# Kernel tuning notes

Measured on AMD Instinct MI355X. Metric: run time of the kernel, lower is better.

## Reference

```python
import jax, jax.numpy as jnp
import numpy as np

B, T, J, V, D, H = 32, 400, 30, 50000, 150, 150
L = 2  # answer_token_len (boundary model: start, end)


def _gru_step(h, x, Wih, Whh, bih, bhh):
    # torch GRUCell semantics
    gi = x @ Wih.T + bih
    gh = h @ Whh.T + bhh
    ir, iz, inn = jnp.split(gi, 3, axis=-1)
    hr, hz, hn = jnp.split(gh, 3, axis=-1)
    r = jax.nn.sigmoid(ir + hr)
    z = jax.nn.sigmoid(iz + hz)
    n = jnp.tanh(inn + r * hn)
    return (1.0 - z) * n + z * h


def _gru_seq(x, Wih, Whh, bih, bhh):
    # x: [B, S, din] -> hidden sequence [B, S, h]
    h0 = jnp.zeros((x.shape[0], Whh.shape[1]), x.dtype)
    def step(h, xt):
        h = _gru_step(h, xt, Wih, Whh, bih, bhh)
        return h, h
    _, hs = jax.lax.scan(step, h0, jnp.swapaxes(x, 0, 1))
    return jnp.swapaxes(hs, 0, 1)


def _forward(context, query,
             E,
             ctx_Wih, ctx_Whh, ctx_bih, ctx_bhh,
             q_Wih, q_Whh, q_bih, q_bhh,
             Wq, Wp, Wr, w, gate_bias, attn_bias,
             m_Wih, m_Whh, m_bih, m_bhh,
             mr_Wih, mr_Whh, mr_bih, mr_bhh,
             ptr_W1, ptr_W2, ptr_v,
             d_Wih, d_Whh, d_bih, d_bhh):
    # encode context and query with GRUs
    Hp = _gru_seq(E[context], ctx_Wih, ctx_Whh, ctx_bih, ctx_bhh)  # [B,T,H]
    Hq = _gru_seq(E[query], q_Wih, q_Whh, q_bih, q_bhh)            # [B,J,H]

    whq = jnp.einsum('bjh,hk->bjk', Hq, Wq)  # precomputed query projection [B,J,H]

    def match_scan(xs, cWih, cWhh, cbih, cbhh):
        # xs: [B,T,H] context encodings (possibly time-reversed)
        def step(h, xt):
            # G_i = tanh(Wq Hq + (Wp p_i + Wr h_{i-1}) + bias)  -> [B,J,H]
            g = jnp.tanh(whq + (xt @ Wp + h @ Wr + gate_bias)[:, None, :])
            a = jax.nn.softmax(g @ w + attn_bias, axis=-1)       # [B,J]
            q = jnp.einsum('bj,bjh->bh', a, Hq)                  # attended query
            z = jnp.concatenate([xt, q], axis=-1)                # [B,2H]
            h = _gru_step(h, z, cWih, cWhh, cbih, cbhh)
            return h, h
        h0 = jnp.zeros((xs.shape[0], xs.shape[2]), xs.dtype)
        _, hs = jax.lax.scan(step, h0, jnp.swapaxes(xs, 0, 1))
        return jnp.swapaxes(hs, 0, 1)  # [B,T,H]

    Hf = match_scan(Hp, m_Wih, m_Whh, m_bih, m_bhh)              # forward direction
    Hb = match_scan(Hp[:, ::-1], mr_Wih, mr_Whh, mr_bih, mr_bhh) # reverse direction (scan order, as original)
    Hr = jnp.concatenate([Hf, Hb], axis=-1)                      # [B,T,2H]
    zero0 = jnp.zeros((Hr.shape[0], 1, Hr.shape[2]), Hr.dtype)   # initial zero state prepended
    Hr = jnp.concatenate([zero0, Hr], axis=1)                    # [B,T+1,2H]

    # boundary pointer network: L attention steps over H_r
    enc = Hr @ ptr_W1
    def ptr_step(h, _):
        s = jnp.tanh(enc + (h @ ptr_W2)[:, None, :]) @ ptr_v     # [B,T+1]
        a = jax.nn.softmax(s, axis=-1)
        c = jnp.einsum('bt,bth->bh', a, Hr)
        h = _gru_step(h, c, d_Wih, d_Whh, d_bih, d_bhh)
        return h, a
    h0 = jnp.zeros((Hr.shape[0], Hr.shape[2]), Hr.dtype)
    _, probs = jax.lax.scan(ptr_step, h0, None, length=L)
    return jnp.swapaxes(probs, 0, 1)  # [B, L, T+1]


def setup_inputs() -> dict:
    key = jax.random.key(0)
    keys = iter(jax.random.split(key, 40))
    p = lambda *s: jax.random.normal(next(keys), s, jnp.float32) * 0.05
    inp = {
        'context': jax.random.randint(next(keys), (B, T), 0, V, dtype=jnp.int32),
        'query': jax.random.randint(next(keys), (B, J), 0, V, dtype=jnp.int32),
        'E': p(V, D),
        'ctx_Wih': p(3 * H, D), 'ctx_Whh': p(3 * H, H), 'ctx_bih': p(3 * H), 'ctx_bhh': p(3 * H),
        'q_Wih': p(3 * H, D), 'q_Whh': p(3 * H, H), 'q_bih': p(3 * H), 'q_bhh': p(3 * H),
        'Wq': p(H, H), 'Wp': p(H, H), 'Wr': p(H, H), 'w': p(H),
        'gate_bias': p(H), 'attn_bias': p(),
        'm_Wih': p(3 * H, 2 * H), 'm_Whh': p(3 * H, H), 'm_bih': p(3 * H), 'm_bhh': p(3 * H),
        'mr_Wih': p(3 * H, 2 * H), 'mr_Whh': p(3 * H, H), 'mr_bih': p(3 * H), 'mr_bhh': p(3 * H),
        'ptr_W1': p(2 * H, 2 * H), 'ptr_W2': p(2 * H, 2 * H), 'ptr_v': p(2 * H),
        'd_Wih': p(6 * H, 2 * H), 'd_Whh': p(6 * H, 2 * H), 'd_bih': p(6 * H), 'd_bhh': p(6 * H),
    }
    return inp


def reference(context, query, E,
              ctx_Wih, ctx_Whh, ctx_bih, ctx_bhh,
              q_Wih, q_Whh, q_bih, q_bhh,
              Wq, Wp, Wr, w, gate_bias, attn_bias,
              m_Wih, m_Whh, m_bih, m_bhh,
              mr_Wih, mr_Whh, mr_bih, mr_bhh,
              ptr_W1, ptr_W2, ptr_v,
              d_Wih, d_Whh, d_bih, d_bhh):
    return _forward(context, query, E,
                    ctx_Wih, ctx_Whh, ctx_bih, ctx_bhh,
                    q_Wih, q_Whh, q_bih, q_bhh,
                    Wq, Wp, Wr, w, gate_bias, attn_bias,
                    m_Wih, m_Whh, m_bih, m_bhh,
                    mr_Wih, mr_Whh, mr_bih, mr_bhh,
                    ptr_W1, ptr_W2, ptr_v,
                    d_Wih, d_Whh, d_bih, d_bhh)
```

## Files before the change

### kernel.cpp

```cpp
#include <hip/hip_runtime.h>
#include <hip/hip_bf16.h>


namespace {

constexpr int NBATCH = 32;
constexpr int TLEN   = 400;
constexpr int JQ     = 30;
constexpr int T1     = 401;

__device__ __forceinline__ float sigm(float x){ return 1.f/(1.f+__expf(-x)); }
__device__ __forceinline__ float tanh_f(float x){
  float e = __expf(-2.f*fabsf(x));
  float t = (1.f-e)/(1.f+e);
  return x < 0.f ? -t : t;
}
__device__ __forceinline__ float bf2f(unsigned short u){
  union { unsigned int i; float f; } c; c.i = ((unsigned int)u)<<16; return c.f;
}
__device__ __forceinline__ float q4max(float4 v){ return fmaxf(fmaxf(v.x,v.y),fmaxf(v.z,v.w)); }
__device__ __forceinline__ float sum4(float4 v){ return (v.x+v.y)+(v.z+v.w); }
__device__ __forceinline__ float4 exp4(float4 v, float m){
  return make_float4(__expf(v.x-m),__expf(v.y-m),__expf(v.z-m),__expf(v.w-m));
}
__device__ __forceinline__ float4 scl4(float4 v, float s){
  return make_float4(v.x*s,v.y*s,v.z*s,v.w*s);
}

__device__ __forceinline__ void bar_lds(){
  asm volatile("s_waitcnt lgkmcnt(0)" ::: "memory");
  __builtin_amdgcn_s_barrier();
}

#define NW 29
struct WDesc { const void* src[NW]; int off[NW+1]; };

__global__ void sniff_kernel(const unsigned int* __restrict__ bits, int* __restrict__ flag){
  __shared__ int cnt;
  if (threadIdx.x==0) cnt = 0;
  __syncthreads();
  int hit = 0;
  #pragma unroll
  for (int i=0;i<4;i++){
    unsigned int w = bits[threadIdx.x*4+i];
    unsigned int b = (w>>8)&0x7Fu;
    if (b==0u || (b>=0x38u && b<=0x3Fu)) hit++;
  }
  atomicAdd(&cnt, hit);
  __syncthreads();
  if (threadIdx.x==0) *flag = (cnt > 768) ? 1 : 0;
}

__global__ void convert_weights_kernel(WDesc d, float* __restrict__ out, const int* __restrict__ flag){
  const int isbf = *flag;
  const int total = d.off[NW];
  for (int e = blockIdx.x*blockDim.x+threadIdx.x; e < total; e += gridDim.x*blockDim.x){
    int j = 0;
    while (e >= d.off[j+1]) j++;
    int i = e - d.off[j];
    out[e] = isbf ? bf2f(((const unsigned short*)d.src[j])[i])
                  : ((const float*)d.src[j])[i];
  }
}

struct PrepArgs {
  const float *ctxWhh, *qWhh, *mWhh, *mrWhh, *Wr;
  const float *ctxWih, *qWih, *mWih, *mrWih;
  float *ctxWhhP, *qWhhP, *s2qCtx, *s2qQ, *WcatF, *WcatR, *s2qF, *s2qR;
  float *extF, *extR, *ctxWihT, *qWihT, *mXfT, *mXrT, *mQfT, *mQrT;
};

__global__ void prep_all_kernel(PrepArgs a){
  const int PN[16] = {68400,68400,21696,21696,91200,91200,24576,24576,
                      13376,13376,67500,67500,67500,67500,67500,67500};
  const int TOT = 843496;
  for (int gid = blockIdx.x*blockDim.x+threadIdx.x; gid < TOT; gid += gridDim.x*blockDim.x){
    int e = gid, t = 0;
    while (e >= PN[t]){ e -= PN[t]; t++; }
    switch (t){
      case 0: case 1: {
        const float* s = (t==0)? a.ctxWhh : a.qWhh;
        float* d = (t==0)? a.ctxWhhP : a.qWhhP;
        int r = e/152, c = e-r*152;
        d[e] = (c<150) ? s[r*150+c] : 0.f;
      } break;
      case 2: case 3: {
        const float* s = (t==2)? a.ctxWhh : a.qWhh;
        float* d = (t==2)? a.s2qCtx : a.s2qQ;
        int q = e/1808, rem = e-q*1808, r = rem/4, p = rem-r*4;
        int c = 104 + 4*q + p;
        d[e] = (r<450 && c<150) ? s[(size_t)r*150+c] : 0.f;
      } break;
      case 4: case 5: {
        const float* s = (t==4)? a.mWhh : a.mrWhh;
        float* d = (t==4)? a.WcatF : a.WcatR;
        int r = e/152, c = e-r*152;
        float v = 0.f;
        if (c < 150) v = (r<450) ? s[(size_t)r*150+c] : a.Wr[(size_t)c*150 + (r-450)];
        d[e] = v;
      } break;
      case 6: case 7: {
        const float* s = (t==6)? a.mWhh : a.mrWhh;
        float* d = (t==6)? a.s2qF : a.s2qR;
        int q = e/2048, rem = e-q*2048, r = rem/4, p = rem-r*4;
        int c = 104 + 4*q + p;
        float v = 0.f;
        if (c < 150) v = (r<450) ? s[(size_t)r*150+c] : a.Wr[(size_t)c*150 + (r-450)];
        d[e] = v;
      } break;
      case 8: case 9: {
        float* d = (t==8)? a.extF : a.extR;
        int q = e/352, rem = e-q*352, ii = rem/4, p = rem-ii*4;
        int c = 4*q + p;
        d[e] = (c<150) ? a.Wr[(size_t)c*150 + 62 + ii] : 0.f;
      } break;
      default: {
        int i2 = e/450, k = e-i2*450;
        const float* s; float* d; int lds_, offs;
        switch (t){
          case 10: s=a.ctxWih; d=a.ctxWihT; lds_=150; offs=0;   break;
          case 11: s=a.qWih;   d=a.qWihT;   lds_=150; offs=0;   break;
          case 12: s=a.mWih;   d=a.mXfT;    lds_=300; offs=0;   break;
          case 13: s=a.mrWih;  d=a.mXrT;    lds_=300; offs=0;   break;
          case 14: s=a.mWih;   d=a.mQfT;    lds_=300; offs=150; break;
          default: s=a.mrWih;  d=a.mQrT;    lds_=300; offs=150; break;
        }
        d[(size_t)i2*450 + k] = s[(size_t)k*lds_ + offs + i2];
      } break;
    }
  }
}

__global__ __launch_bounds__(512) void rowproj16_kernel(
    const float* __restrict__ Xrows,
    const int* __restrict__ gather, const void* __restrict__ Etab, const int* __restrict__ bfflag,
    const float* __restrict__ W, const float* __restrict__ bias,
    float* __restrict__ out, int rows, int K, int inner, int ldw, int ldo)
{
  __shared__ __align__(16) float xs[16][304];
  const int r0 = blockIdx.x*16;
  int nr = rows - r0; if (nr > 16) nr = 16;
  if (nr <= 0) return;
  const int isbf = gather ? *bfflag : 0;
  for (int e = threadIdx.x; e < nr*inner; e += 512){
    int r = e/inner, i = e - r*inner;
    float v;
    if (gather){
      size_t base = (size_t)gather[r0+r]*inner + i;
      v = isbf ? bf2f(((const unsigned short*)Etab)[base]) : ((const float*)Etab)[base];
    } else {
      v = Xrows[(size_t)(r0+r)*inner + i];
    }
    xs[r][i] = v;
  }
  __syncthreads();
  for (int k = threadIdx.x; k < K; k += 512){
    float b0 = bias ? bias[k] : 0.f;
    float acc[16];
    #pragma unroll
    for (int r=0;r<16;r++) acc[r] = b0;
    int i = 0;
    for (; i+4 <= inner; i += 4){
      float w0 = W[(size_t)i*ldw + k];
      float w1 = W[(size_t)(i+1)*ldw + k];
      float w2 = W[(size_t)(i+2)*ldw + k];
      float w3 = W[(size_t)(i+3)*ldw + k];
      #pragma unroll
      for (int r=0;r<16;r++){
        float4 xv = *(const float4*)&xs[r][i];
        acc[r] = fmaf(xv.x, w0, acc[r]);
        acc[r] = fmaf(xv.y, w1, acc[r]);
        acc[r] = fmaf(xv.z, w2, acc[r]);
        acc[r] = fmaf(xv.w, w3, acc[r]);
      }
    }
    for (; i < inner; i++){
      float wv = W[(size_t)i*ldw + k];
      #pragma unroll
      for (int r=0;r<16;r++) acc[r] = fmaf(xs[r][i], wv, acc[r]);
    }
    for (int r=0;r<nr;r++) out[(size_t)(r0+r)*ldo + k] = acc[r];
  }
  for (int k = K + threadIdx.x; k < ldo; k += 512)
    for (int r=0;r<nr;r++) out[(size_t)(r0+r)*ldo + k] = 0.f;
}

__device__ __forceinline__ void rowproj_one(
    const float xs[16][152], int nr, int r0,
    const float* __restrict__ W, const float* __restrict__ bias,
    float* __restrict__ out, int K, int ldw, int ldo)
{
  for (int k = threadIdx.x; k < K; k += 512){
    float b0 = bias ? bias[k] : 0.f;
    float acc[16];
    #pragma unroll
    for (int r=0;r<16;r++) acc[r] = b0;
    int i = 0;
    for (; i+4 <= 148; i += 4){
      float w0 = W[(size_t)i*ldw + k];
      float w1 = W[(size_t)(i+1)*ldw + k];
      float w2 = W[(size_t)(i+2)*ldw + k];
      float w3 = W[(size_t)(i+3)*ldw + k];
      #pragma unroll
      for (int r=0;r<16;r++){
        float4 xv = *(const float4*)&xs[r][i];
        acc[r] = fmaf(xv.x, w0, acc[r]);
        acc[r] = fmaf(xv.y, w1, acc[r]);
        acc[r] = fmaf(xv.z, w2, acc[r]);
        acc[r] = fmaf(xv.w, w3, acc[r]);
      }
    }
    {
      float w0 = W[(size_t)148*ldw + k];
      float w1 = W[(size_t)149*ldw + k];
      #pragma unroll
      for (int r=0;r<16;r++){
        acc[r] = fmaf(xs[r][148], w0, acc[r]);
        acc[r] = fmaf(xs[r][149], w1, acc[r]);
      }
    }
    for (int r=0;r<nr;r++) out[(size_t)(r0+r)*ldo + k] = acc[r];
  }
  for (int k = K + threadIdx.x; k < ldo; k += 512)
    for (int r=0;r<nr;r++) out[(size_t)(r0+r)*ldo + k] = 0.f;
}

__global__ __launch_bounds__(512) void rowproj16_3_kernel(
    const float* __restrict__ X, int rows,
    const float* __restrict__ W0, const float* __restrict__ b0, float* __restrict__ o0,
    int K0, int ldw0, int ldo0,
    const float* __restrict__ W1, const float* __restrict__ b1, float* __restrict__ o1,
    int K1, int ldw1, int ldo1,
    const float* __restrict__ W2, const float* __restrict__ b2, float* __restrict__ o2,
    int K2, int ldw2, int ldo2)
{
  __shared__ __align__(16) float xs[16][152];
  const int r0 = blockIdx.x*16;
  int nr = rows - r0; if (nr > 16) nr = 16;
  if (nr <= 0) return;
  for (int e = threadIdx.x; e < nr*150; e += 512){
    int r = e/150, i = e - r*150;
    xs[r][i] = X[(size_t)(r0+r)*150 + i];
  }
  if (threadIdx.x < 32){
    int r = threadIdx.x/2, i = 150 + (threadIdx.x&1);
    if (r < 16) xs[r][i] = 0.f;
  }
  __syncthreads();
  rowproj_one(xs, nr, r0, W0, b0, o0, K0, ldw0, ldo0);
  rowproj_one(xs, nr, r0, W1, b1, o1, K1, ldw1, ldo1);
  rowproj_one(xs, nr, r0, W2, b2, o2, K2, ldw2, ldo2);
}

#define R26(M) M(0) M(1) M(2) M(3) M(4) M(5) M(6) M(7) M(8) M(9) M(10) M(11) \
               M(12) M(13) M(14) M(15) M(16) M(17) M(18) M(19) M(20) M(21) \
               M(22) M(23) M(24) M(25)
#define R12(M) M(26) M(27) M(28) M(29) M(30) M(31) M(32) M(33) M(34) M(35) \
               M(36) M(37)
#define DECW(i) float4 w##i;
#define LDW(i)  w##i = wrow4[i];
#define LDW2(i) w##i = s2q4[(i-26)*s2stride + s2r];
#define FMAW(i) { float4 hq = h4[i]; \
  acc0 = fmaf(hq.x, w##i.x, acc0); acc1 = fmaf(hq.y, w##i.y, acc1); \
  acc2 = fmaf(hq.z, w##i.z, acc2); acc3 = fmaf(hq.w, w##i.w, acc3); }

__global__ __launch_bounds__(512, 2) void gru_scan_kernel(
    const float* __restrict__ gi0, const float* __restrict__ Wp0,
    const float* __restrict__ s2q0, const float* __restrict__ bh0,
    float* __restrict__ H0, int S0,
    const float* __restrict__ gi1, const float* __restrict__ Wp1,
    const float* __restrict__ s2q1, const float* __restrict__ bh1,
    float* __restrict__ H1, int S1)
{
  const int blk = blockIdx.x;
  const float* gi; const float* Wpad; const float* s2qG; const float* bh; float* Hs; int S;
  if (blk < 32){ gi = gi0 + (size_t)blk*S0*450;  Wpad = Wp0; s2qG = s2q0; bh = bh0;
                 Hs = H0 + (size_t)blk*S0*150;   S = S0; }
  else         { int bb = blk-32;
                 gi = gi1 + (size_t)bb*S1*450;   Wpad = Wp1; s2qG = s2q1; bh = bh1;
                 Hs = H1 + (size_t)bb*S1*150;    S = S1; }
  __shared__ __align__(16) float h[152];
  __shared__ float gh[452];
  const int tid = threadIdx.x;

  R26(DECW) R12(DECW)
  float br = 0.f;
  {
    const float4* wrow4 = (const float4*)(Wpad + (size_t)((tid<450)?tid:0)*152);
    R26(LDW)
    const float4* s2q4 = (const float4*)s2qG;
    const int s2stride = 452; const int s2r = (tid<452) ? tid : 0;
    R12(LDW2)
    if (tid<450) br = bh[tid];
  }
  if (tid < 152) h[tid] = 0.f;
  __syncthreads();
  const float4* h4 = (const float4*)h;

  for (int t=0;t<S;t++){
    float g0=0.f,g1=0.f,g2=0.f;
    if (tid < 150){
      const float* gg = gi + (size_t)t*450;
      g0 = gg[tid]; g1 = gg[150+tid]; g2 = gg[300+tid];
    }
    if (tid < 450){
      float acc0=br, acc1=0.f, acc2=0.f, acc3=0.f;
      R26(FMAW) R12(FMAW)
      gh[tid] = (acc0+acc2)+(acc1+acc3);
    }
    bar_lds();
    if (tid < 150){
      float r = sigm(g0 + gh[tid]);
      float z = sigm(g1 + gh[150+tid]);
      float n = tanh_f(g2 + r*gh[300+tid]);
      float hn = (1.f-z)*n + z*h[tid];
      h[tid] = hn;
      Hs[(size_t)t*150 + tid] = hn;
    }
    bar_lds();
  }
}

__global__ void zero_hr0_kernel(float* __restrict__ Hr){
  int idx = blockIdx.x*blockDim.x + threadIdx.x;
  if (idx < NBATCH*300){
    int b = idx/300, k = idx - 300*b;
    Hr[(size_t)b*T1*300 + k] = 0.f;
  }
}

__global__ __launch_bounds__(512, 2) void match_scan_kernel(
    const float* __restrict__ pWp,
    const float* __restrict__ whq,
    const float* __restrict__ giXf,
    const float* __restrict__ giXr,
    const float* __restrict__ Pf,
    const float* __restrict__ Pr,
    const float* __restrict__ WcatF, const float* __restrict__ WcatR,
    const float* __restrict__ s2qF,  const float* __restrict__ s2qR,
    const float* __restrict__ extF,  const float* __restrict__ extR,
    const float* __restrict__ m_bhh, const float* __restrict__ mr_bhh,
    const float* __restrict__ wvec,
    float* __restrict__ Hr)
{
  const int b   = blockIdx.x;
  const int dir = blockIdx.y;
  const float* giX  = dir ? giXr : giXf;
  const float* P    = dir ? Pr   : Pf;
  const float* Wcat = dir ? WcatR : WcatF;
  const float* s2qG = dir ? s2qR  : s2qF;
  const float* extG = dir ? extR  : extF;
  const float* bhh  = dir ? mr_bhh : m_bhh;

  __shared__ float4 extW[3344];
  __shared__ __align__(16) float PsT[15000];
  __shared__ __align__(16) float whqS[JQ*152];
  __shared__ __align__(16) float wrP[760];
  __shared__ __align__(16) float h[152];
  __shared__ float ghsRaw[512];
  __shared__ __align__(16) float pwS[152];
  __shared__ __align__(16) float wlS[152];
  __shared__ __align__(16) float sc[32];
  const int tid  = threadIdx.x;
  const int lane = tid & 63;
  const int wv   = tid >> 6;
  const int er   = (tid < 440) ? (tid % 88) : 0;
  const int kg   = (tid < 440) ? (tid / 88) : 0;

  R26(DECW) R12(DECW)
  float br;
  {
    const float4* wrow4 = (const float4*)(Wcat + (size_t)tid*152);
    R26(LDW)
    const float4* s2q4 = (const float4*)s2qG;
    const int s2stride = 512; const int s2r = tid;
    R12(LDW2)
    br = (tid < 450) ? bhh[tid] : 0.f;
  }
  for (int e=tid; e<3344; e+=512) extW[e] = ((const float4*)extG)[e];
  {
    const float4* wq4 = (const float4*)(whq + (size_t)b*JQ*152);
    for (int e=tid; e<JQ*38; e+=512) ((float4*)whqS)[e] = wq4[e];
  }
  for (int e=tid; e<15000; e+=512) PsT[e] = 0.f;
  for (int e=tid; e<760;   e+=512) wrP[e] = 0.f;
  if (tid < 152){
    h[tid] = 0.f;
    wlS[tid] = (tid<150) ? wvec[tid] : 0.f;
  }
  if (tid >= 30 && tid < 32) sc[tid] = -1e30f;
  __syncthreads();
  {
    const float* Pb = P + (size_t)b*JQ*452;
    for (int e=tid; e<JQ*452; e+=512){
      int j = e/452, kk = e - j*452;
      if (kk < 450){
        int g = kk/150, k = kk - g*150;
        PsT[k*100 + g*32 + j] = Pb[e];
      }
    }
  }
  __syncthreads();
  const float4* h4 = (const float4*)h;
  const float4* wrP4 = (const float4*)wrP;

  for (int t=0;t<TLEN;t++){
    const int tt = dir ? (TLEN-1-t) : t;

    float gv0=0.f, gv1=0.f, gv2=0.f;
    if (tid < 150){
      const float* g = giX + ((size_t)b*TLEN + tt)*452;
      gv0 = g[tid]; gv1 = g[150+tid]; gv2 = g[300+tid];
    }
    float4 pwv;
    if (tid >= 440 && tid < 478)
      pwv = ((const float4*)(pWp + ((size_t)b*TLEN + tt)*152))[tid-440];

    {
      float acc0=br, acc1=0.f, acc2=0.f, acc3=0.f;
      R26(FMAW) R12(FMAW)
      float v = (acc0+acc2)+(acc1+acc3);
      ghsRaw[tid] = v;
      if (tid >= 450) wrP[tid-450] = v;
    }
    if (tid < 440){
      float e0=0.f, e1=0.f;
      #pragma unroll
      for (int j=0;j<8;j++){
        int q = kg*8+j;
        if (q < 38){
          float4 wq = extW[q*88+er]; float4 hq = h4[q];
          e0 = fmaf(hq.x,wq.x,e0); e1 = fmaf(hq.y,wq.y,e1);
          e0 = fmaf(hq.z,wq.z,e0); e1 = fmaf(hq.w,wq.w,e1);
        }
      }
      wrP[kg*152 + 62 + er] = e0+e1;
    }
    if (tid >= 440 && tid < 478) ((float4*)pwS)[tid-440] = pwv;
    bar_lds();

    {
      float4 b4 = make_float4(0.f,0.f,0.f,0.f);
      const bool bl = (lane < 38);
      if (bl){
        float4 pw4 = ((const float4*)pwS)[lane];
        float4 s0 = wrP4[lane],        s1 = wrP4[38+lane];
        float4 s2 = wrP4[76+lane],     s3 = wrP4[114+lane];
        float4 s4 = wrP4[152+lane];
        b4.x = pw4.x + s0.x+s1.x+s2.x+s3.x+s4.x;
        b4.y = pw4.y + s0.y+s1.y+s2.y+s3.y+s4.y;
        b4.z = pw4.z + s0.z+s1.z+s2.z+s3.z+s4.z;
        b4.w = pw4.w + s0.w+s1.w+s2.w+s3.w+s4.w;
      }
      #pragma unroll
      for (int jj=0;jj<4;jj++){
        int j = wv + 8*jj;
        float a = 0.f;
        if (j < JQ && bl){
          float4 q4 = ((const float4*)whqS)[j*38 + lane];
          float4 w4 = ((const float4*)wlS)[lane];
          a = w4.x*tanh_f(q4.x+b4.x);
          a = fmaf(w4.y, tanh_f(q4.y+b4.y), a);
          a = fmaf(w4.z, tanh_f(q4.z+b4.z), a);
          a = fmaf(w4.w, tanh_f(q4.w+b4.w), a);
        }
        #pragma unroll
        for (int off=32; off; off>>=1) a += __shfl_down(a, off);
        if (j < JQ && lane==0) sc[j] = a;
      }
    }
    bar_lds();

    if (tid < 192){
      const float4* sc4 = (const float4*)sc;
      float4 s0=sc4[0], s1=sc4[1], s2=sc4[2], s3=sc4[3];
      float4 s4=sc4[4], s5=sc4[5], s6=sc4[6], s7=sc4[7];
      float m = fmaxf(fmaxf(fmaxf(q4max(s0),q4max(s1)),fmaxf(q4max(s2),q4max(s3))),
                      fmaxf(fmaxf(q4max(s4),q4max(s5)),fmaxf(q4max(s6),q4max(s7))));
      float4 a0=exp4(s0,m), a1=exp4(s1,m), a2=exp4(s2,m), a3=exp4(s3,m);
      float4 a4=exp4(s4,m), a5=exp4(s5,m), a6=exp4(s6,m), a7=exp4(s7,m);
      float su = ((sum4(a0)+sum4(a1))+(sum4(a2)+sum4(a3)))
               + ((sum4(a4)+sum4(a5))+(sum4(a6)+sum4(a7)));
      float inv = 1.f/su;
      a0=scl4(a0,inv); a1=scl4(a1,inv); a2=scl4(a2,inv); a3=scl4(a3,inv);
      a4=scl4(a4,inv); a5=scl4(a5,inv); a6=scl4(a6,inv); a7=scl4(a7,inv);
      const int k = (tid < 150) ? tid : 0;
      const float4* Pk = (const float4*)(PsT + k*100);
      float accr = gv0, accz = gv1, accn = gv2;
      #define ACC1(acc,P4,A4){ float4 p=P4; \
        acc=fmaf(A4.x,p.x,acc); acc=fmaf(A4.y,p.y,acc); \
        acc=fmaf(A4.z,p.z,acc); acc=fmaf(A4.w,p.w,acc); }
      #define ACCG(acc,g){ ACC1(acc,Pk[g*8+0],a0) ACC1(acc,Pk[g*8+1],a1) \
        ACC1(acc,Pk[g*8+2],a2) ACC1(acc,Pk[g*8+3],a3) ACC1(acc,Pk[g*8+4],a4) \
        ACC1(acc,Pk[g*8+5],a5) ACC1(acc,Pk[g*8+6],a6) ACC1(acc,Pk[g*8+7],a7) }
      ACCG(accr,0) ACCG(accz,1) ACCG(accn,2)
      #undef ACC1
      #undef ACCG
      if (tid < 150){
        float r = sigm(accr + ghsRaw[tid]);
        float z = sigm(accz + ghsRaw[150+tid]);
        float n = tanh_f(accn + r*ghsRaw[300+tid]);
        float hn = (1.f-z)*n + z*h[tid];
        h[tid] = hn;
        Hr[((size_t)b*T1 + (t+1))*300 + dir*150 + tid] = hn;
      }
    }
    bar_lds();
  }
}

__global__ __launch_bounds__(512,2) void ptr_scan_kernel(
    const float* __restrict__ enc, const float* __restrict__ Hr,
    const float* __restrict__ W2, const float* __restrict__ pv,
    const float* __restrict__ dWih, const float* __restrict__ dWhh,
    const float* __restrict__ dbih, const float* __restrict__ dbhh,
    void* __restrict__ outv, const int* __restrict__ flag)
{
  const int b = blockIdx.x;
  const int tid = threadIdx.x;
  const int isbf = *flag;
  __shared__ float h[300], hW2[300], sl[T1], al[T1], c[300];
  __shared__ float gis[900], ghs[900];
  __shared__ float vl[300];
  __shared__ float red[8];
  if (tid < 300){ h[tid] = 0.f; vl[tid] = pv[tid]; }
  __syncthreads();
  for (int l=0;l<2;l++){
    if (tid < 300){
      float a0=0.f,a1=0.f;
      for (int i=0;i<300;i+=2){
        a0 += h[i]  *W2[(size_t)i*300+tid];
        a1 += h[i+1]*W2[(size_t)(i+1)*300+tid];
      }
      hW2[tid] = a0+a1;
    }
    __syncthreads();
    {
      const int wv = tid>>6, lane = tid&63;
      for (int t=wv; t<T1; t+=8){
        const float* er = enc + ((size_t)b*T1 + t)*300;
        float acc = 0.f;
        for (int k=lane; k<300; k+=64) acc += vl[k]*tanh_f(er[k] + hW2[k]);
        #pragma unroll
        for (int off=32; off; off>>=1) acc += __shfl_down(acc, off);
        if (lane==0) sl[t] = acc;
      }
    }
    __syncthreads();
    {
      float v = (tid < T1) ? sl[tid] : -1e30f;
      float m = v;
      #pragma unroll
      for (int off=32; off; off>>=1) m = fmaxf(m, __shfl_down(m, off));
      if ((tid&63)==0) red[tid>>6] = m;
      __syncthreads();
      float bm = fmaxf(fmaxf(fmaxf(red[0],red[1]),fmaxf(red[2],red[3])),
                       fmaxf(fmaxf(red[4],red[5]),fmaxf(red[6],red[7])));
      float e = (tid < T1) ? __expf(v-bm) : 0.f;
      float su = e;
      #pragma unroll
      for (int off=32; off; off>>=1) su += __shfl_down(su, off);
      __syncthreads();
      if ((tid&63)==0) red[tid>>6] = su;
      __syncthreads();
      float bs = red[0]+red[1]+red[2]+red[3]+red[4]+red[5]+red[6]+red[7];
      if (tid < T1){
        float a = e/bs;
        al[tid] = a;
        size_t oi = ((size_t)b*2 + l)*T1 + tid;
        if (isbf) ((__hip_bfloat16*)outv)[oi] = __float2bfloat16(a);
        else      ((float*)outv)[oi] = a;
      }
    }
    __syncthreads();
    if (tid < 300){
      float acc = 0.f;
      for (int t=0;t<T1;t++) acc += al[t]*Hr[((size_t)b*T1 + t)*300 + tid];
      c[tid] = acc;
    }
    __syncthreads();
    for (int k=tid; k<900; k+=blockDim.x){
      const float* wi = dWih + (size_t)k*300;
      const float* wh = dWhh + (size_t)k*300;
      float a0 = dbih[k], a1 = dbhh[k];
      for (int i=0;i<300;i++){ a0 += c[i]*wi[i]; a1 += h[i]*wh[i]; }
      gis[k] = a0; ghs[k] = a1;
    }
    __syncthreads();
    if (tid < 300){
      float r = sigm(gis[tid] + ghs[tid]);
      float z = sigm(gis[300+tid] + ghs[300+tid]);
      float n = tanh_f(gis[600+tid] + r*ghs[600+tid]);
      h[tid] = (1.f-z)*n + z*h[tid];
    }
    __syncthreads();
  }
}

}

extern "C" void kernel_launch(void* const* d_in, const int* in_sizes, int n_in,
                              void* d_out, int out_size, void* d_ws, size_t ws_size,
                              hipStream_t stream)
{
  (void)in_sizes; (void)n_in; (void)out_size; (void)ws_size;
  float* ws = (float*)d_ws;
  int* flag = (int*)d_ws;

  static const int wsz[NW] = {
    67500,67500,450,450,
    67500,67500,450,450,
    22500,22500,22500,150,150,1,
    135000,67500,450,450,
    135000,67500,450,450,
    90000,90000,300,
    270000,270000,900,900
  };
  WDesc desc;
  int cum = 0;
  for (int j=0;j<NW;j++){ desc.src[j] = d_in[3+j]; desc.off[j] = cum; cum += wsz[j]; }
  desc.off[NW] = cum;

  float* WB = ws + 16;
  const float* P_ctx_Wih = WB + desc.off[0];
  const float* P_ctx_Whh = WB + desc.off[1];
  const float* P_ctx_bih = WB + desc.off[2];
  const float* P_ctx_bhh = WB + desc.off[3];
  const float* P_q_Wih   = WB + desc.off[4];
  const float* P_q_Whh   = WB + desc.off[5];
  const float* P_q_bih   = WB + desc.off[6];
  const float* P_q_bhh   = WB + desc.off[7];
  const float* P_Wq      = WB + desc.off[8];
  const float* P_Wp      = WB + desc.off[9];
  const float* P_Wr      = WB + desc.off[10];
  const float* P_w       = WB + desc.off[11];
  const float* P_gb      = WB + desc.off[12];
  const float* P_m_Wih   = WB + desc.off[14];
  const float* P_m_Whh   = WB + desc.off[15];
  const float* P_m_bih   = WB + desc.off[16];
  const float* P_m_bhh   = WB + desc.off[17];
  const float* P_mr_Wih  = WB + desc.off[18];
  const float* P_mr_Whh  = WB + desc.off[19];
  const float* P_mr_bih  = WB + desc.off[20];
  const float* P_mr_bhh  = WB + desc.off[21];
  const float* P_W1      = WB + desc.off[22];
  const float* P_W2      = WB + desc.off[23];
  const float* P_pv      = WB + desc.off[24];
  const float* P_dWih    = WB + desc.off[25];
  const float* P_dWhh    = WB + desc.off[26];
  const float* P_dbih    = WB + desc.off[27];
  const float* P_dbhh    = WB + desc.off[28];

  size_t p = 16 + 1468512;
  float* ctxWhhP = ws + p; p += 68400;
  float* qWhhP   = ws + p; p += 68400;
  float* s2qCtx  = ws + p; p += 21696;
  float* s2qQ    = ws + p; p += 21696;
  float* WcatF   = ws + p; p += 91200;
  float* WcatR   = ws + p; p += 91200;
  float* s2qF    = ws + p; p += 24576;
  float* s2qR    = ws + p; p += 24576;
  float* extFg   = ws + p; p += 13376;
  float* extRg   = ws + p; p += 13376;
  float* ctxWihT = ws + p; p += 67500;
  float* qWihT   = ws + p; p += 67500;
  float* mXfT    = ws + p; p += 67500;
  float* mXrT    = ws + p; p += 67500;
  float* mQfT    = ws + p; p += 67500;
  float* mQrT    = ws + p; p += 67500;

  float* ctx_gi = ws + p; p += 5760000;
  float* q_gi   = ws + p; p += 432000;
  float* HpB    = ws + p; p += 1920000;
  float* HqB    = ws + p; p += 144000;
  float* whqB   = ws + p; p += 145920;
  float* PfB    = ws + p; p += 433920;
  float* PrB    = ws + p; p += 433920;
  float* pWpB   = ws + p; p += 1945600;
  float* giXfB  = ws + p; p += 5785600;
  float* giXrB  = ws + p; p += 5785600;
  float* HrB    = ws + p; p += 3849600;
  float* encB   = ctx_gi;

  sniff_kernel<<<1,256,0,stream>>>((const unsigned int*)d_in[2], flag);
  convert_weights_kernel<<<512,256,0,stream>>>(desc, WB, flag);
  {
    PrepArgs a;
    a.ctxWhh = P_ctx_Whh; a.qWhh = P_q_Whh; a.mWhh = P_m_Whh; a.mrWhh = P_mr_Whh;
    a.Wr = P_Wr; a.ctxWih = P_ctx_Wih; a.qWih = P_q_Wih; a.mWih = P_m_Wih; a.mrWih = P_mr_Wih;
    a.ctxWhhP = ctxWhhP; a.qWhhP = qWhhP; a.s2qCtx = s2qCtx; a.s2qQ = s2qQ;
    a.WcatF = WcatF; a.WcatR = WcatR; a.s2qF = s2qF; a.s2qR = s2qR;
    a.extF = extFg; a.extR = extRg; a.ctxWihT = ctxWihT; a.qWihT = qWihT;
    a.mXfT = mXfT; a.mXrT = mXrT; a.mQfT = mQfT; a.mQrT = mQrT;
    prep_all_kernel<<<2048,256,0,stream>>>(a);
  }

  rowproj16_kernel<<<800,512,0,stream>>>(nullptr,(const int*)d_in[0], d_in[2], flag,
                                         ctxWihT, P_ctx_bih, ctx_gi, 12800,450,150,450,450);
  rowproj16_kernel<<<60,512,0,stream>>>(nullptr,(const int*)d_in[1], d_in[2], flag,
                                        qWihT, P_q_bih, q_gi, 960,450,150,450,450);

  gru_scan_kernel<<<64,512,0,stream>>>(ctx_gi, ctxWhhP, s2qCtx, P_ctx_bhh, HpB, 400,
                                       q_gi,   qWhhP,   s2qQ,   P_q_bhh,   HqB, 30);

  rowproj16_3_kernel<<<60,512,0,stream>>>(HqB, 960,
      P_Wq, nullptr, whqB, 150, 150, 152,
      mQfT, nullptr, PfB, 450, 450, 452,
      mQrT, nullptr, PrB, 450, 450, 452);
  rowproj16_3_kernel<<<800,512,0,stream>>>(HpB, 12800,
      P_Wp, P_gb, pWpB, 150, 150, 152,
      mXfT, P_m_bih, giXfB, 450, 450, 452,
      mXrT, P_mr_bih, giXrB, 450, 450, 452);

  zero_hr0_kernel<<<(NBATCH*300+511)/512,512,0,stream>>>(HrB);
  match_scan_kernel<<<dim3(NBATCH,2),512,0,stream>>>(pWpB, whqB, giXfB, giXrB,
                                                     PfB, PrB, WcatF, WcatR,
                                                     s2qF, s2qR, extFg, extRg,
                                                     P_m_bhh, P_mr_bhh, P_w, HrB);

  rowproj16_kernel<<<802,512,0,stream>>>(HrB,nullptr,nullptr,nullptr, P_W1, nullptr,
                                         encB, 12832,300,300,300,300);
  ptr_scan_kernel<<<32,512,0,stream>>>(encB, HrB, P_W2, P_pv,
                                       P_dWih, P_dWhh, P_dbih, P_dbhh, d_out, flag);
}
```

Baseline: 3.197 ms.

## Keep extension weights in registers and use DPP wave reduction for scores

```diff
diff --git a/kernel.cpp b/kernel.cpp
--- a/kernel.cpp
+++ b/kernel.cpp
@@ -25,6 +25,18 @@
 }
 __device__ __forceinline__ float4 scl4(float4 v, float s){
   return make_float4(v.x*s,v.y*s,v.z*s,v.w*s);
+}
+
+__device__ __forceinline__ float wave_sum64(float a){
+  float x = a, y = a;
+  asm volatile("v_permlane32_swap_b32 %0, %1" : "+v"(x), "+v"(y));
+  a = x + y;
+  a += __int_as_float(__builtin_amdgcn_ds_swizzle(__float_as_int(a), 0x401F));
+  a += __int_as_float(__builtin_amdgcn_update_dpp(0, __float_as_int(a), 0x118, 0xF, 0xF, true));
+  a += __int_as_float(__builtin_amdgcn_update_dpp(0, __float_as_int(a), 0x114, 0xF, 0xF, true));
+  a += __int_as_float(__builtin_amdgcn_update_dpp(0, __float_as_int(a), 0x112, 0xF, 0xF, true));
+  a += __int_as_float(__builtin_amdgcn_update_dpp(0, __float_as_int(a), 0x111, 0xF, 0xF, true));
+  return a;
 }
 
 __device__ __forceinline__ void bar_lds(){
@@ -257,12 +269,19 @@
                M(22) M(23) M(24) M(25)
 #define R12(M) M(26) M(27) M(28) M(29) M(30) M(31) M(32) M(33) M(34) M(35) \
                M(36) M(37)
+#define E8(M)  M(0) M(1) M(2) M(3) M(4) M(5) M(6) M(7)
 #define DECW(i) float4 w##i;
 #define LDW(i)  w##i = wrow4[i];
 #define LDW2(i) w##i = s2q4[(i-26)*s2stride + s2r];
 #define FMAW(i) { float4 hq = h4[i]; \
   acc0 = fmaf(hq.x, w##i.x, acc0); acc1 = fmaf(hq.y, w##i.y, acc1); \
   acc2 = fmaf(hq.z, w##i.z, acc2); acc3 = fmaf(hq.w, w##i.w, acc3); }
+#define DECE(j) float4 ex##j;
+#define LDE(j)  { int q = kg*8+j; \
+  ex##j = (tid<440 && q<38) ? extG4[q*88+er] : make_float4(0.f,0.f,0.f,0.f); }
+#define FMAE(j) { float4 hq = h4[kg*8+j]; \
+  f0 = fmaf(hq.x, ex##j.x, f0); f1 = fmaf(hq.y, ex##j.y, f1); \
+  f0 = fmaf(hq.z, ex##j.z, f0); f1 = fmaf(hq.w, ex##j.w, f1); }
 
 __global__ __launch_bounds__(512, 2) void gru_scan_kernel(
     const float* __restrict__ gi0, const float* __restrict__ Wp0,
@@ -352,11 +371,10 @@
   const float* extG = dir ? extR  : extF;
   const float* bhh  = dir ? mr_bhh : m_bhh;
 
-  __shared__ float4 extW[3344];
   __shared__ __align__(16) float PsT[15000];
   __shared__ __align__(16) float whqS[JQ*152];
   __shared__ __align__(16) float wrP[760];
-  __shared__ __align__(16) float h[152];
+  __shared__ __align__(16) float h[160];
   __shared__ float ghsRaw[512];
   __shared__ __align__(16) float pwS[152];
   __shared__ __align__(16) float wlS[152];
@@ -377,17 +395,16 @@
     R12(LDW2)
     br = (tid < 450) ? bhh[tid] : 0.f;
   }
-  for (int e=tid; e<3344; e+=512) extW[e] = ((const float4*)extG)[e];
+  const float4* extG4 = (const float4*)extG;
+  E8(DECE) E8(LDE)
   {
     const float4* wq4 = (const float4*)(whq + (size_t)b*JQ*152);
     for (int e=tid; e<JQ*38; e+=512) ((float4*)whqS)[e] = wq4[e];
   }
   for (int e=tid; e<15000; e+=512) PsT[e] = 0.f;
   for (int e=tid; e<760;   e+=512) wrP[e] = 0.f;
-  if (tid < 152){
-    h[tid] = 0.f;
-    wlS[tid] = (tid<150) ? wvec[tid] : 0.f;
-  }
+  if (tid < 160) h[tid] = 0.f;
+  if (tid < 152) wlS[tid] = (tid<150) ? wvec[tid] : 0.f;
   if (tid >= 30 && tid < 32) sc[tid] = -1e30f;
   __syncthreads();
   {
@@ -423,18 +440,10 @@
       ghsRaw[tid] = v;
       if (tid >= 450) wrP[tid-450] = v;
     }
-    if (tid < 440){
-      float e0=0.f, e1=0.f;
-      #pragma unroll
-      for (int j=0;j<8;j++){
-        int q = kg*8+j;
-        if (q < 38){
-          float4 wq = extW[q*88+er]; float4 hq = h4[q];
-          e0 = fmaf(hq.x,wq.x,e0); e1 = fmaf(hq.y,wq.y,e1);
-          e0 = fmaf(hq.z,wq.z,e0); e1 = fmaf(hq.w,wq.w,e1);
-        }
-      }
-      wrP[kg*152 + 62 + er] = e0+e1;
+    {
+      float f0=0.f, f1=0.f;
+      E8(FMAE)
+      if (tid < 440) wrP[kg*152 + 62 + er] = f0+f1;
     }
     if (tid >= 440 && tid < 478) ((float4*)pwS)[tid-440] = pwv;
     bar_lds();
@@ -464,8 +473,7 @@
           a = fmaf(w4.z, tanh_f(q4.z+b4.z), a);
           a = fmaf(w4.w, tanh_f(q4.w+b4.w), a);
         }
-        #pragma unroll
-        for (int off=32; off; off>>=1) a += __shfl_down(a, off);
+        a = wave_sum64(a);
         if (j < JQ && lane==0) sc[j] = a;
       }
     }
```

Result: no change. 3.259 ms (+2.0%).
